# Optimization experiments

Hardware: AMD Instinct MI355X
Metric: run time of the kernel (lower is better)

The kernel has to match this reference:

```python
import jax, jax.numpy as jnp
import numpy as np

NEG = -1e9  # mask value for non-edges (matches masked_fill(-inf) numerically-safely)
SLOPE = 0.2  # LeakyReLU negative slope in GraphAttentionLayer


def gat_layer(x, W, a_l, a_r, adj, n_heads):
    """One GraphAttentionLayer (eval mode, is_concat=True).
    e[i,j,h] = leakyrelu(a_l . g[i,h] + a_r . g[j,h])  (attn Linear split into halves)
    softmax over j masked by adj, then aggregate neighbors.
    """
    n = x.shape[0]
    g = (x @ W).reshape(n, n_heads, -1)          # [n, h, f]
    el = jnp.einsum('ihf,f->ih', g, a_l)          # score contribution of node i
    er = jnp.einsum('jhf,f->jh', g, a_r)          # score contribution of node j
    e = jax.nn.leaky_relu(el[:, None, :] + er[None, :, :], SLOPE)  # [n, n, h]
    e = jnp.where(adj[:, :, None] != 0, e, NEG)
    a = jax.nn.softmax(e, axis=1)                 # softmax over neighbors j
    out = jnp.einsum('ijh,jhf->ihf', a, g)        # weighted aggregation
    return out.reshape(n, -1)                     # concat heads


def setup_inputs() -> dict:
    key = jax.random.key(0)
    ks = jax.random.split(key, 8)
    N, IN, HID, OUT, H = 2048, 512, 256, 128, 8
    x = jax.random.normal(ks[0], (N, IN), dtype=jnp.float32)
    adj = jax.random.randint(ks[1], (N, N), 0, 2, dtype=jnp.int32)
    adj = adj.at[jnp.arange(N), jnp.arange(N)].set(1)  # self loops: no empty softmax rows
    s = 0.05
    W1 = jax.random.normal(ks[2], (IN, HID), dtype=jnp.float32) * s
    a1_l = jax.random.normal(ks[3], (HID // H,), dtype=jnp.float32) * s
    a1_r = jax.random.normal(ks[4], (HID // H,), dtype=jnp.float32) * s
    W2 = jax.random.normal(ks[5], (HID, OUT), dtype=jnp.float32) * s
    a2_l = jax.random.normal(ks[6], (OUT,), dtype=jnp.float32) * s
    a2_r = jax.random.normal(ks[7], (OUT,), dtype=jnp.float32) * s
    return {"x": x, "W1": W1, "a1_l": a1_l, "a1_r": a1_r,
            "W2": W2, "a2_l": a2_l, "a2_r": a2_r, "adj_mat": adj}


def reference(x, W1, a1_l, a1_r, W2, a2_l, a2_r, adj_mat):
    # eval mode: nn.Dropout is identity
    h = gat_layer(x, W1, a1_l, a1_r, adj_mat, n_heads=8)
    h = jax.nn.elu(h)
    out = gat_layer(h, W2, a2_l, a2_r, adj_mat, n_heads=1)
    return out
```

## Files before the change

kernel.cpp:

```cpp
#include <hip/hip_runtime.h>
#include <hip/hip_bf16.h>

#define NN 2048
typedef unsigned short u16;
typedef unsigned long long u64;
typedef __attribute__((ext_vector_type(8))) short short8;
typedef __attribute__((ext_vector_type(4))) float f32x4;

__device__ __forceinline__ unsigned bfb(float x) {
    unsigned u = __float_as_uint(x);
    return (u + 0x7FFFu + ((u >> 16) & 1u)) >> 16;
}
__device__ __forceinline__ unsigned pk2(float a, float b) {
    unsigned r;
    asm("v_cvt_pk_bf16_f32 %0, %1, %2" : "=v"(r) : "v"(a), "v"(b));
    return r;
}

__global__ __launch_bounds__(256) void gemm1(const float* __restrict__ x,
                                             const float* __restrict__ W1,
                                             const int* __restrict__ adj,
                                             const float* __restrict__ al,
                                             const float* __restrict__ ar,
                                             u16* __restrict__ GT,
                                             float* __restrict__ el,
                                             float* __restrict__ ert,
                                             u64* __restrict__ ab) {
    const int rt = blockIdx.x, cs = blockIdx.y;
    const int t = threadIdx.x;
    if (cs >= 8) {
        const int b = (cs - 8) * 128 + rt;
        const int r0 = b * 8;
        const int lane = t & 63;
#pragma unroll 4
        for (int k = 0; k < 64; ++k) {
            int tl = k * 256 + t;
            int W = tl >> 6;
            int rl = W >> 5, jw = W & 31;
            int a = adj[(size_t)(r0 + rl) * NN + jw * 64 + lane];
            u64 mk = __ballot(a != 0);
            if (lane == 0) ab[(size_t)(r0 + rl) * 32 + jw] = mk;
        }
        return;
    }
    const int i0 = rt * 16;
    const int lane = t & 63, w = t >> 6;
    const int q = lane >> 4, n = lane & 15;
    const int ct = w & 1, kh = w >> 1;
    __shared__ __align__(16) u16 As[16][520];
    __shared__ __align__(16) u16 Bs[32][520];
    __shared__ float osh[2][16][16];
    __shared__ float pel[2][16], per_[2][16];

    {
        const float4* xs = (const float4*)(x + (size_t)i0 * 512);
#pragma unroll
        for (int j = 0; j < 8; ++j) {
            float4 v = xs[j * 256 + t];
            int off = (j * 256 + t) * 4;
            int r = off >> 9, k = off & 511;
            uint2 o;
            o.x = pk2(v.x, v.y);
            o.y = pk2(v.z, v.w);
            *(uint2*)&As[r][k] = o;
        }
    }
    {
        const int cl = t & 31, kr0 = t >> 5;
#pragma unroll 4
        for (int it = 0; it < 64; ++it) {
            int k = it * 8 + kr0;
            Bs[cl][k] = (u16)bfb(W1[(size_t)k * 256 + cs * 32 + cl]);
        }
    }
    __syncthreads();

    const u16* apl = &As[n][kh * 256 + q * 8];
    const u16* bpl = &Bs[ct * 16 + n][kh * 256 + q * 8];
    f32x4 acc = {0.f, 0.f, 0.f, 0.f};
#pragma unroll
    for (int ks = 0; ks < 8; ++ks) {
        short8 a = *(const short8*)(apl + ks * 32);
        short8 b = *(const short8*)(bpl + ks * 32);
        acc = __builtin_amdgcn_mfma_f32_16x16x32_bf16(a, b, acc, 0, 0, 0);
    }
    __syncthreads();
    if (kh == 1) {
#pragma unroll
        for (int r = 0; r < 4; ++r) osh[ct][q * 4 + r][n] = acc[r];
    }
    __syncthreads();
    if (kh == 0) {
#pragma unroll
        for (int r = 0; r < 4; ++r) acc[r] += osh[ct][q * 4 + r][n];
        uint2 g0;
        g0.x = pk2(acc[0], acc[1]);
        g0.y = pk2(acc[2], acc[3]);
        *(uint2*)&GT[(size_t)(cs * 32 + ct * 16 + n) * NN + i0 + q * 4] = g0;
        const float alv = al[ct * 16 + n], arv = ar[ct * 16 + n];
#pragma unroll
        for (int r = 0; r < 4; ++r) {
            float ve = acc[r] * alv, vr = acc[r] * arv;
#pragma unroll
            for (int off = 1; off <= 8; off <<= 1) {
                ve += __shfl_xor(ve, off);
                vr += __shfl_xor(vr, off);
            }
            if (n == 0) { pel[ct][q * 4 + r] = ve; per_[ct][q * 4 + r] = vr; }
        }
    }
    __syncthreads();
    if (t < 16) {
        el[(size_t)(i0 + t) * 8 + cs] = pel[0][t] + pel[1][t];
        ert[(size_t)cs * NN + i0 + t] = per_[0][t] + per_[1][t];
    }
}

__global__ __launch_bounds__(256) void gemm2(const u16* __restrict__ A,
                                             const float* __restrict__ W2,
                                             const float* __restrict__ al,
                                             const float* __restrict__ ar,
                                             u16* __restrict__ GT,
                                             float* __restrict__ el2p,
                                             float* __restrict__ er2p) {
    const int i0 = blockIdx.x * 16, cs = blockIdx.y;
    const int t = threadIdx.x, lane = t & 63, w = t >> 6;
    const int q = lane >> 4, n = lane & 15;
    const int ct = w & 1, kh = w >> 1;
    __shared__ __align__(16) u16 As[16][264];
    __shared__ __align__(16) u16 Bs[32][264];
    __shared__ float osh[2][16][16];
    __shared__ float pel[2][16], per_[2][16];

    {
        const uint2* hs = (const uint2*)(A + (size_t)i0 * 256);
#pragma unroll
        for (int j = 0; j < 4; ++j) {
            uint2 v = hs[j * 256 + t];
            int off = (j * 256 + t) * 4;
            int r = off >> 8, k = off & 255;
            *(uint2*)&As[r][k] = v;
        }
    }
    {
        const int cl = t & 31, kr0 = t >> 5;
#pragma unroll 4
        for (int it = 0; it < 32; ++it) {
            int k = it * 8 + kr0;
            Bs[cl][k] = (u16)bfb(W2[(size_t)k * 128 + cs * 32 + cl]);
        }
    }
    __syncthreads();

    const u16* apl = &As[n][kh * 128 + q * 8];
    const u16* bpl = &Bs[ct * 16 + n][kh * 128 + q * 8];
    f32x4 acc = {0.f, 0.f, 0.f, 0.f};
#pragma unroll
    for (int ks = 0; ks < 4; ++ks) {
        short8 a = *(const short8*)(apl + ks * 32);
        short8 b = *(const short8*)(bpl + ks * 32);
        acc = __builtin_amdgcn_mfma_f32_16x16x32_bf16(a, b, acc, 0, 0, 0);
    }
    __syncthreads();
    if (kh == 1) {
#pragma unroll
        for (int r = 0; r < 4; ++r) osh[ct][q * 4 + r][n] = acc[r];
    }
    __syncthreads();
    if (kh == 0) {
#pragma unroll
        for (int r = 0; r < 4; ++r) acc[r] += osh[ct][q * 4 + r][n];
        uint2 g0;
        g0.x = pk2(acc[0], acc[1]);
        g0.y = pk2(acc[2], acc[3]);
        *(uint2*)&GT[(size_t)(cs * 32 + ct * 16 + n) * NN + i0 + q * 4] = g0;
        const float alv = al[cs * 32 + ct * 16 + n], arv = ar[cs * 32 + ct * 16 + n];
#pragma unroll
        for (int r = 0; r < 4; ++r) {
            float ve = acc[r] * alv, vr = acc[r] * arv;
#pragma unroll
            for (int off = 1; off <= 8; off <<= 1) {
                ve += __shfl_xor(ve, off);
                vr += __shfl_xor(vr, off);
            }
            if (n == 0) { pel[ct][q * 4 + r] = ve; per_[ct][q * 4 + r] = vr; }
        }
    }
    __syncthreads();
    if (t < 16) {
        el2p[(size_t)cs * NN + i0 + t] = pel[0][t] + pel[1][t];
        er2p[(size_t)cs * NN + i0 + t] = per_[0][t] + per_[1][t];
    }
}

__global__ __launch_bounds__(512, 4) void attn1(const float* __restrict__ el,
                                                const float* __restrict__ ert,
                                                const unsigned* __restrict__ ab32,
                                                const u16* __restrict__ gbt,
                                                u16* __restrict__ hbb) {
    const int rt = blockIdx.x, sec = blockIdx.y;
    const int i0 = rt * 16, h0 = sec * 2;
    const int t = threadIdx.x, lane = t & 63, w = t >> 6;
    const int q = lane >> 4, n = lane & 15;
    const int m = t >> 5, jq = t & 31;
    const int hl = w >> 2, ch = (w >> 1) & 1, kf2 = w & 1;

    __shared__ u16 ersb[2][2048];
    __shared__ __align__(16) u16 pl[2][2][16][264];
    __shared__ unsigned absh[16][64];
    __shared__ float psum_sh[16][2];
    __shared__ float osh[2][2][16][16];
    __shared__ float wmax[2][8];
    __shared__ float mxsh[2];

    float4 v0 = *(const float4*)(ert + (size_t)h0 * NN + t * 4);
    float4 v1 = *(const float4*)(ert + (size_t)(h0 + 1) * NN + t * 4);
    uint2 c0, c1;
    c0.x = pk2(v0.x, v0.y); c0.y = pk2(v0.z, v0.w);
    c1.x = pk2(v1.x, v1.y); c1.y = pk2(v1.z, v1.w);
    *(uint2*)&ersb[0][t * 4] = c0;
    *(uint2*)&ersb[1][t * 4] = c1;
    float m0 = fmaxf(fmaxf(v0.x, v0.y), fmaxf(v0.z, v0.w));
    float m1 = fmaxf(fmaxf(v1.x, v1.y), fmaxf(v1.z, v1.w));
#pragma unroll
    for (int off = 32; off; off >>= 1) {
        m0 = fmaxf(m0, __shfl_xor(m0, off));
        m1 = fmaxf(m1, __shfl_xor(m1, off));
    }
    if (lane == 0) { wmax[0][w] = m0; wmax[1][w] = m1; }
    for (int c = t; c < 1024; c += 512)
        absh[c >> 6][c & 63] = ab32[(size_t)(i0 + (c >> 6)) * 64 + (c & 63)];
    __syncthreads();
    if (t < 2) {
        float mm = wmax[t][0];
#pragma unroll
        for (int ww = 1; ww < 8; ++ww) mm = fmaxf(mm, wmax[t][ww]);
        mxsh[t] = mm;
    }
    __syncthreads();

    float elv[2], mxv[2], ps[2];
#pragma unroll
    for (int h = 0; h < 2; ++h) {
        float e = el[(size_t)(i0 + m) * 8 + h0 + h];
        elv[h] = e;
        float mm = e + mxsh[h];
        mxv[h] = fmaxf(mm, 0.2f * mm);
        ps[h] = 0.f;
    }

    auto stage = [&](int tl, int nb) {
#pragma unroll
        for (int sub = 0; sub < 2; ++sub) {
            unsigned word = absh[m][tl * 8 + sub * 4 + (jq >> 3)];
            unsigned bits = (word >> ((jq & 7) * 4)) & 0xFu;
            const int jo = tl * 256 + sub * 128 + jq * 4;
            uint2 raw0 = *(const uint2*)&ersb[0][jo];
            uint2 raw1 = *(const uint2*)&ersb[1][jo];
#pragma unroll
            for (int h = 0; h < 2; ++h) {
                uint2 raw = h ? raw1 : raw0;
                float e0 = __uint_as_float(raw.x << 16);
                float e1 = __uint_as_float(raw.x & 0xFFFF0000u);
                float e2 = __uint_as_float(raw.y << 16);
                float e3 = __uint_as_float(raw.y & 0xFFFF0000u);
                float s0 = elv[h] + e0, s1 = elv[h] + e1, s2 = elv[h] + e2, s3 = elv[h] + e3;
                s0 = fmaxf(s0, 0.2f * s0) - mxv[h];
                s1 = fmaxf(s1, 0.2f * s1) - mxv[h];
                s2 = fmaxf(s2, 0.2f * s2) - mxv[h];
                s3 = fmaxf(s3, 0.2f * s3) - mxv[h];
                float p0 = (bits & 1u) ? __expf(s0) : 0.f;
                float p1 = (bits & 2u) ? __expf(s1) : 0.f;
                float p2 = (bits & 4u) ? __expf(s2) : 0.f;
                float p3 = (bits & 8u) ? __expf(s3) : 0.f;
                ps[h] += (p0 + p1) + (p2 + p3);
                uint2 pkv;
                pkv.x = pk2(p0, p1);
                pkv.y = pk2(p2, p3);
                *(uint2*)&pl[nb][h][m][sub * 128 + jq * 4] = pkv;
            }
        }
    };

    const int col = sec * 64 + hl * 32 + ch * 16 + n;
    const u16* gb = gbt + (size_t)col * NN + kf2 * 128 + q * 8;
    short8 bc0 = *(const short8*)gb;
    short8 bc1 = *(const short8*)(gb + 32);
    short8 bc2 = *(const short8*)(gb + 64);
    short8 bc3 = *(const short8*)(gb + 96);
    f32x4 acc = {0.f, 0.f, 0.f, 0.f};

    stage(0, 0);
    __syncthreads();

    for (int tile = 0; tile < 8; ++tile) {
        short8 bn0 = bc0, bn1 = bc1, bn2 = bc2, bn3 = bc3;
        if (tile < 7) {
            const u16* gq = gb + (tile + 1) * 256;
            bn0 = *(const short8*)gq;
            bn1 = *(const short8*)(gq + 32);
            bn2 = *(const short8*)(gq + 64);
            bn3 = *(const short8*)(gq + 96);
        }
        const u16* ap = &pl[tile & 1][hl][n][kf2 * 128 + q * 8];
        short8 a0 = *(const short8*)ap;
        short8 a1 = *(const short8*)(ap + 32);
        short8 a2 = *(const short8*)(ap + 64);
        short8 a3 = *(const short8*)(ap + 96);
        acc = __builtin_amdgcn_mfma_f32_16x16x32_bf16(a0, bc0, acc, 0, 0, 0);
        acc = __builtin_amdgcn_mfma_f32_16x16x32_bf16(a1, bc1, acc, 0, 0, 0);
        acc = __builtin_amdgcn_mfma_f32_16x16x32_bf16(a2, bc2, acc, 0, 0, 0);
        acc = __builtin_amdgcn_mfma_f32_16x16x32_bf16(a3, bc3, acc, 0, 0, 0);
        if (tile < 7) stage(tile + 1, (tile + 1) & 1);
        bc0 = bn0; bc1 = bn1; bc2 = bn2; bc3 = bn3;
        __syncthreads();
    }

#pragma unroll
    for (int h = 0; h < 2; ++h) {
        float v = ps[h];
#pragma unroll
        for (int off = 16; off; off >>= 1) v += __shfl_down(v, off, 32);
        if (jq == 0) psum_sh[m][h] = v;
    }
    if (kf2 == 1) {
#pragma unroll
        for (int r = 0; r < 4; ++r) osh[hl][ch][q * 4 + r][n] = acc[r];
    }
    __syncthreads();
    if (kf2 == 0) {
#pragma unroll
        for (int r = 0; r < 4; ++r) {
            int mr = q * 4 + r;
            float o = (acc[r] + osh[hl][ch][mr][n]) / psum_sh[mr][hl];
            o = o > 0.f ? o : (__expf(o) - 1.f);
            hbb[(size_t)(i0 + mr) * 256 + col] = (u16)bfb(o);
        }
    }
}

__global__ __launch_bounds__(512) void attn2(const float* __restrict__ el2p,
                                             const float* __restrict__ er2p,
                                             const unsigned* __restrict__ ab32,
                                             const u16* __restrict__ gbt,
                                             float* __restrict__ out) {
    const int rt = blockIdx.x, sec = blockIdx.y;
    const int i0 = rt * 16;
    const int t = threadIdx.x, lane = t & 63, w = t >> 6;
    const int q = lane >> 4, n = lane & 15;
    const int m = t >> 5, jq = t & 31;
    const int ct = w >> 1, kf2 = w & 1;

    __shared__ u16 ersb[2048];
    __shared__ __align__(16) u16 pl[2][16][264];
    __shared__ unsigned absh[16][64];
    __shared__ float psum_sh[16];
    __shared__ float osh[4][16][16];
    __shared__ float wmax[8];
    __shared__ float mxsh;

    float4 a0 = *(const float4*)(er2p + t * 4);
    float4 a1 = *(const float4*)(er2p + NN + t * 4);
    float4 a2 = *(const float4*)(er2p + 2 * NN + t * 4);
    float4 a3 = *(const float4*)(er2p + 3 * NN + t * 4);
    float4 v0;
    v0.x = ((a0.x + a1.x) + (a2.x + a3.x));
    v0.y = ((a0.y + a1.y) + (a2.y + a3.y));
    v0.z = ((a0.z + a1.z) + (a2.z + a3.z));
    v0.w = ((a0.w + a1.w) + (a2.w + a3.w));
    uint2 c0;
    c0.x = pk2(v0.x, v0.y); c0.y = pk2(v0.z, v0.w);
    *(uint2*)&ersb[t * 4] = c0;
    float m0 = fmaxf(fmaxf(v0.x, v0.y), fmaxf(v0.z, v0.w));
#pragma unroll
    for (int off = 32; off; off >>= 1) m0 = fmaxf(m0, __shfl_xor(m0, off));
    if (lane == 0) wmax[w] = m0;
    for (int c = t; c < 1024; c += 512)
        absh[c >> 6][c & 63] = ab32[(size_t)(i0 + (c >> 6)) * 64 + (c & 63)];
    __syncthreads();
    if (t == 0) {
        float mm = wmax[0];
#pragma unroll
        for (int ww = 1; ww < 8; ++ww) mm = fmaxf(mm, wmax[ww]);
        mxsh = mm;
    }
    __syncthreads();

    const float elv = el2p[i0 + m] + el2p[NN + i0 + m] + el2p[2 * NN + i0 + m] + el2p[3 * NN + i0 + m];
    float mm2 = elv + mxsh;
    const float mxv = fmaxf(mm2, 0.2f * mm2);
    float ps = 0.f;

    auto stage = [&](int tl, int nb) {
#pragma unroll
        for (int sub = 0; sub < 2; ++sub) {
            unsigned word = absh[m][tl * 8 + sub * 4 + (jq >> 3)];
            unsigned bits = (word >> ((jq & 7) * 4)) & 0xFu;
            const int jo = tl * 256 + sub * 128 + jq * 4;
            uint2 raw = *(const uint2*)&ersb[jo];
            float e0 = __uint_as_float(raw.x << 16);
            float e1 = __uint_as_float(raw.x & 0xFFFF0000u);
            float e2 = __uint_as_float(raw.y << 16);
            float e3 = __uint_as_float(raw.y & 0xFFFF0000u);
            float s0 = elv + e0, s1 = elv + e1, s2 = elv + e2, s3 = elv + e3;
            s0 = fmaxf(s0, 0.2f * s0) - mxv;
            s1 = fmaxf(s1, 0.2f * s1) - mxv;
            s2 = fmaxf(s2, 0.2f * s2) - mxv;
            s3 = fmaxf(s3, 0.2f * s3) - mxv;
            float p0 = (bits & 1u) ? __expf(s0) : 0.f;
            float p1 = (bits & 2u) ? __expf(s1) : 0.f;
            float p2 = (bits & 4u) ? __expf(s2) : 0.f;
            float p3 = (bits & 8u) ? __expf(s3) : 0.f;
            ps += (p0 + p1) + (p2 + p3);
            uint2 pkv;
            pkv.x = pk2(p0, p1);
            pkv.y = pk2(p2, p3);
            *(uint2*)&pl[nb][m][sub * 128 + jq * 4] = pkv;
        }
    };

    const int col = sec * 64 + ct * 16 + n;
    const u16* gb = gbt + (size_t)col * NN + kf2 * 128 + q * 8;
    short8 bc0 = *(const short8*)gb;
    short8 bc1 = *(const short8*)(gb + 32);
    short8 bc2 = *(const short8*)(gb + 64);
    short8 bc3 = *(const short8*)(gb + 96);
    f32x4 acc = {0.f, 0.f, 0.f, 0.f};

    stage(0, 0);
    __syncthreads();

    for (int tile = 0; tile < 8; ++tile) {
        short8 bn0 = bc0, bn1 = bc1, bn2 = bc2, bn3 = bc3;
        if (tile < 7) {
            const u16* gq = gb + (tile + 1) * 256;
            bn0 = *(const short8*)gq;
            bn1 = *(const short8*)(gq + 32);
            bn2 = *(const short8*)(gq + 64);
            bn3 = *(const short8*)(gq + 96);
        }
        const u16* ap = &pl[tile & 1][n][kf2 * 128 + q * 8];
        short8 a0v = *(const short8*)ap;
        short8 a1v = *(const short8*)(ap + 32);
        short8 a2v = *(const short8*)(ap + 64);
        short8 a3v = *(const short8*)(ap + 96);
        acc = __builtin_amdgcn_mfma_f32_16x16x32_bf16(a0v, bc0, acc, 0, 0, 0);
        acc = __builtin_amdgcn_mfma_f32_16x16x32_bf16(a1v, bc1, acc, 0, 0, 0);
        acc = __builtin_amdgcn_mfma_f32_16x16x32_bf16(a2v, bc2, acc, 0, 0, 0);
        acc = __builtin_amdgcn_mfma_f32_16x16x32_bf16(a3v, bc3, acc, 0, 0, 0);
        if (tile < 7) stage(tile + 1, (tile + 1) & 1);
        bc0 = bn0; bc1 = bn1; bc2 = bn2; bc3 = bn3;
        __syncthreads();
    }

#pragma unroll
    for (int off = 16; off; off >>= 1) ps += __shfl_down(ps, off, 32);
    if (jq == 0) psum_sh[m] = ps;
    if (kf2 == 1) {
#pragma unroll
        for (int r = 0; r < 4; ++r) osh[ct][q * 4 + r][n] = acc[r];
    }
    __syncthreads();
    if (kf2 == 0) {
#pragma unroll
        for (int r = 0; r < 4; ++r) {
            int mr = q * 4 + r;
            out[(size_t)(i0 + mr) * 128 + col] = (acc[r] + osh[ct][mr][n]) / psum_sh[mr];
        }
    }
}

extern "C" void kernel_launch(void* const* d_in, const int* in_sizes, int n_in,
                              void* d_out, int out_size, void* d_ws, size_t ws_size,
                              hipStream_t stream) {
    const float* x   = (const float*)d_in[0];
    const float* W1  = (const float*)d_in[1];
    const float* a1l = (const float*)d_in[2];
    const float* a1r = (const float*)d_in[3];
    const float* W2  = (const float*)d_in[4];
    const float* a2l = (const float*)d_in[5];
    const float* a2r = (const float*)d_in[6];
    const int* adj = (const int*)d_in[7];

    char* p = (char*)d_ws;
    unsigned* abits = (unsigned*)p;  p += (size_t)NN * 64 * 4;
    u16* gbt1  = (u16*)p;            p += (size_t)256 * NN * 2;
    u16* hbb   = (u16*)p;            p += (size_t)NN * 256 * 2;
    u16* gbt2  = (u16*)p;            p += (size_t)128 * NN * 2;
    float* el1 = (float*)p;          p += (size_t)NN * 8 * 4;
    float* ert1 = (float*)p;         p += (size_t)8 * NN * 4;
    float* el2p = (float*)p;         p += (size_t)4 * NN * 4;
    float* er2p = (float*)p;         p += (size_t)4 * NN * 4;

    gemm1<<<dim3(128, 10), 256, 0, stream>>>(x, W1, adj, a1l, a1r, gbt1, el1, ert1, (u64*)abits);
    attn1<<<dim3(128, 4), 512, 0, stream>>>(el1, ert1, abits, gbt1, hbb);

    gemm2<<<dim3(128, 4), 256, 0, stream>>>(hbb, W2, a2l, a2r, gbt2, el2p, er2p);
    attn2<<<dim3(128, 2), 512, 0, stream>>>(el2p, er2p, abits, gbt2, (float*)d_out);
}
```

Measured before the change: 139.2 us.

## Fold adjacency bitmask packing into GEMM1 blocks and swizzle LDS tiles

Removes the separate adjacency-packing blocks from gemm1. Every GEMM block now issues its share of adjacency loads up front, keeps them in registers while it stages x and W1, then ballots and writes the bitmask. Both GEMMs load W as float4 and XOR-swizzle the As/Bs shared tiles to cut bank conflicts, and the redundant syncthreads after the MFMA loop is dropped. This overlaps the adjacency read latency with GEMM staging, at the cost of 16 extra live registers per thread.

```diff
diff --git a/kernel.cpp b/kernel.cpp
--- a/kernel.cpp
+++ b/kernel.cpp
@@ -27,30 +27,23 @@
                                              float* __restrict__ ert,
                                              u64* __restrict__ ab) {
     const int rt = blockIdx.x, cs = blockIdx.y;
-    const int t = threadIdx.x;
-    if (cs >= 8) {
-        const int b = (cs - 8) * 128 + rt;
-        const int r0 = b * 8;
-        const int lane = t & 63;
-#pragma unroll 4
-        for (int k = 0; k < 64; ++k) {
-            int tl = k * 256 + t;
-            int W = tl >> 6;
-            int rl = W >> 5, jw = W & 31;
-            int a = adj[(size_t)(r0 + rl) * NN + jw * 64 + lane];
-            u64 mk = __ballot(a != 0);
-            if (lane == 0) ab[(size_t)(r0 + rl) * 32 + jw] = mk;
-        }
-        return;
-    }
     const int i0 = rt * 16;
-    const int lane = t & 63, w = t >> 6;
+    const int t = threadIdx.x, lane = t & 63, w = t >> 6;
     const int q = lane >> 4, n = lane & 15;
     const int ct = w & 1, kh = w >> 1;
     __shared__ __align__(16) u16 As[16][520];
     __shared__ __align__(16) u16 Bs[32][520];
     __shared__ float osh[2][16][16];
     __shared__ float pel[2][16], per_[2][16];
+
+    const int b = cs * 128 + rt;
+    const int u0 = b * 64 + w * 16;
+    int av[16];
+#pragma unroll
+    for (int it = 0; it < 16; ++it) {
+        int u = u0 + it;
+        av[it] = adj[(size_t)(u >> 5) * NN + (u & 31) * 64 + lane];
+    }
 
     {
         const float4* xs = (const float4*)(x + (size_t)i0 * 512);
@@ -62,29 +55,38 @@
             uint2 o;
             o.x = pk2(v.x, v.y);
             o.y = pk2(v.z, v.w);
-            *(uint2*)&As[r][k] = o;
+            *(uint2*)&As[r][k ^ ((r & 7) << 3)] = o;
         }
     }
     {
-        const int cl = t & 31, kr0 = t >> 5;
-#pragma unroll 4
-        for (int it = 0; it < 64; ++it) {
-            int k = it * 8 + kr0;
-            Bs[cl][k] = (u16)bfb(W1[(size_t)k * 256 + cs * 32 + cl]);
-        }
-    }
-    __syncthreads();
-
-    const u16* apl = &As[n][kh * 256 + q * 8];
-    const u16* bpl = &Bs[ct * 16 + n][kh * 256 + q * 8];
+        const int c4 = (t & 7) * 4, kq = t >> 3;
+#pragma unroll 8
+        for (int pass = 0; pass < 16; ++pass) {
+            int k = pass * 32 + kq;
+            float4 v = *(const float4*)(W1 + (size_t)k * 256 + cs * 32 + c4);
+            Bs[c4 + 0][k ^ (((c4 + 0) & 7) << 3)] = (u16)bfb(v.x);
+            Bs[c4 + 1][k ^ (((c4 + 1) & 7) << 3)] = (u16)bfb(v.y);
+            Bs[c4 + 2][k ^ (((c4 + 2) & 7) << 3)] = (u16)bfb(v.z);
+            Bs[c4 + 3][k ^ (((c4 + 3) & 7) << 3)] = (u16)bfb(v.w);
+        }
+    }
+#pragma unroll
+    for (int it = 0; it < 16; ++it) {
+        u64 mk = __ballot(av[it] != 0);
+        int u = u0 + it;
+        if (lane == 0) ab[(size_t)(u >> 5) * 32 + (u & 31)] = mk;
+    }
+    __syncthreads();
+
+    const int an = n, bn = ct * 16 + n;
+    const int k0 = kh * 256 + q * 8;
     f32x4 acc = {0.f, 0.f, 0.f, 0.f};
 #pragma unroll
     for (int ks = 0; ks < 8; ++ks) {
-        short8 a = *(const short8*)(apl + ks * 32);
-        short8 b = *(const short8*)(bpl + ks * 32);
-        acc = __builtin_amdgcn_mfma_f32_16x16x32_bf16(a, b, acc, 0, 0, 0);
-    }
-    __syncthreads();
+        short8 a = *(const short8*)&As[an][(k0 + ks * 32) ^ ((an & 7) << 3)];
+        short8 bb = *(const short8*)&Bs[bn][(k0 + ks * 32) ^ ((bn & 7) << 3)];
+        acc = __builtin_amdgcn_mfma_f32_16x16x32_bf16(a, bb, acc, 0, 0, 0);
+    }
     if (kh == 1) {
 #pragma unroll
         for (int r = 0; r < 4; ++r) osh[ct][q * 4 + r][n] = acc[r];
@@ -139,29 +141,32 @@
             uint2 v = hs[j * 256 + t];
             int off = (j * 256 + t) * 4;
             int r = off >> 8, k = off & 255;
-            *(uint2*)&As[r][k] = v;
+            *(uint2*)&As[r][k ^ ((r & 7) << 3)] = v;
         }
     }
     {
-        const int cl = t & 31, kr0 = t >> 5;
-#pragma unroll 4
-        for (int it = 0; it < 32; ++it) {
-            int k = it * 8 + kr0;
-            Bs[cl][k] = (u16)bfb(W2[(size_t)k * 128 + cs * 32 + cl]);
-        }
-    }
-    __syncthreads();
-
-    const u16* apl = &As[n][kh * 128 + q * 8];
-    const u16* bpl = &Bs[ct * 16 + n][kh * 128 + q * 8];
+        const int c4 = (t & 7) * 4, kq = t >> 3;
+#pragma unroll 8
+        for (int pass = 0; pass < 8; ++pass) {
+            int k = pass * 32 + kq;
+            float4 v = *(const float4*)(W2 + (size_t)k * 128 + cs * 32 + c4);
+            Bs[c4 + 0][k ^ (((c4 + 0) & 7) << 3)] = (u16)bfb(v.x);
+            Bs[c4 + 1][k ^ (((c4 + 1) & 7) << 3)] = (u16)bfb(v.y);
+            Bs[c4 + 2][k ^ (((c4 + 2) & 7) << 3)] = (u16)bfb(v.z);
+            Bs[c4 + 3][k ^ (((c4 + 3) & 7) << 3)] = (u16)bfb(v.w);
+        }
+    }
+    __syncthreads();
+
+    const int an = n, bn = ct * 16 + n;
+    const int k0 = kh * 128 + q * 8;
     f32x4 acc = {0.f, 0.f, 0.f, 0.f};
 #pragma unroll
     for (int ks = 0; ks < 4; ++ks) {
-        short8 a = *(const short8*)(apl + ks * 32);
-        short8 b = *(const short8*)(bpl + ks * 32);
-        acc = __builtin_amdgcn_mfma_f32_16x16x32_bf16(a, b, acc, 0, 0, 0);
-    }
-    __syncthreads();
+        short8 a = *(const short8*)&As[an][(k0 + ks * 32) ^ ((an & 7) << 3)];
+        short8 bb = *(const short8*)&Bs[bn][(k0 + ks * 32) ^ ((bn & 7) << 3)];
+        acc = __builtin_amdgcn_mfma_f32_16x16x32_bf16(a, bb, acc, 0, 0, 0);
+    }
     if (kh == 1) {
 #pragma unroll
         for (int r = 0; r < 4; ++r) osh[ct][q * 4 + r][n] = acc[r];
@@ -492,7 +497,7 @@
     float* el2p = (float*)p;         p += (size_t)4 * NN * 4;
     float* er2p = (float*)p;         p += (size_t)4 * NN * 4;
 
-    gemm1<<<dim3(128, 10), 256, 0, stream>>>(x, W1, adj, a1l, a1r, gbt1, el1, ert1, (u64*)abits);
+    gemm1<<<dim3(128, 8), 256, 0, stream>>>(x, W1, adj, a1l, a1r, gbt1, el1, ert1, (u64*)abits);
     attn1<<<dim3(128, 4), 512, 0, stream>>>(el1, ert1, abits, gbt1, hbb);
 
     gemm2<<<dim3(128, 4), 256, 0, stream>>>(hbb, W2, a2l, a2r, gbt2, el2p, er2p);
```

Result: faster. 123.8 us (-11.1%).
